# Kernel tuning notes

Hardware: AMD Instinct MI355X
Metric: run time of the kernel (lower is better)

The kernel has to match this reference:

```python
import jax, jax.numpy as jnp
import numpy as np

DIM = 2048
N_HEADS = 16
N_KV_HEADS = 4
HEAD_DIM = DIM // N_HEADS  # 128
ROPE_BASE = 10000.0
B, S = 4, 2048


def rope_tables(seq_len, head_dim, base, dtype):
    half = head_dim // 2
    inv_freq = 1.0 / (base ** (jnp.arange(0, head_dim, 2, dtype=jnp.float32) / head_dim))
    t = jnp.arange(seq_len, dtype=jnp.float32)
    freqs = jnp.outer(t, inv_freq)  # [S, half]
    return jnp.cos(freqs).astype(dtype), jnp.sin(freqs).astype(dtype)


def apply_rotary(x, cos, sin):
    # x: [B, H, S, D]; cos/sin: [S, D/2] broadcast over B,H
    half = x.shape[-1] // 2
    x1, x2 = x[..., :half], x[..., half:]
    return jnp.concatenate((x1 * cos + x2 * sin, x1 * -sin + x2 * cos), axis=-1)


def setup_inputs() -> dict:
    key = jax.random.key(0)
    ks = jax.random.split(key, 5)
    sc = 1.0 / np.sqrt(DIM)
    return {
        "x": jax.random.normal(ks[0], (B, S, DIM), dtype=jnp.float32),
        "wq": jax.random.normal(ks[1], (DIM, DIM), dtype=jnp.float32) * sc,
        "wk": jax.random.normal(ks[2], (N_KV_HEADS * HEAD_DIM, DIM), dtype=jnp.float32) * sc,
        "wv": jax.random.normal(ks[3], (N_KV_HEADS * HEAD_DIM, DIM), dtype=jnp.float32) * sc,
        "wo": jax.random.normal(ks[4], (DIM, DIM), dtype=jnp.float32) * sc,
    }


def reference(x, wq, wk, wv, wo):
    bsz, seqlen, _ = x.shape
    q = jnp.einsum("bsd,ed->bse", x, wq).reshape(bsz, seqlen, N_HEADS, HEAD_DIM).transpose(0, 2, 1, 3)
    k = jnp.einsum("bsd,ed->bse", x, wk).reshape(bsz, seqlen, N_KV_HEADS, HEAD_DIM).transpose(0, 2, 1, 3)
    v = jnp.einsum("bsd,ed->bse", x, wv).reshape(bsz, seqlen, N_KV_HEADS, HEAD_DIM).transpose(0, 2, 1, 3)

    cos, sin = rope_tables(seqlen, HEAD_DIM, ROPE_BASE, q.dtype)
    q = apply_rotary(q, cos, sin)
    k = apply_rotary(k, cos, sin)

    rep = N_HEADS // N_KV_HEADS
    if rep > 1:
        k = jnp.repeat(k, rep, axis=1)
        v = jnp.repeat(v, rep, axis=1)

    scale = 1.0 / np.sqrt(HEAD_DIM)
    logits = jnp.einsum("bhqd,bhkd->bhqk", q, k) * scale
    causal = jnp.tril(jnp.ones((seqlen, seqlen), dtype=bool))
    logits = jnp.where(causal, logits, jnp.finfo(logits.dtype).min)
    attn = jax.nn.softmax(logits, axis=-1)
    y = jnp.einsum("bhqk,bhkd->bhqd", attn, v)

    y = y.transpose(0, 2, 1, 3).reshape(bsz, seqlen, DIM)
    return jnp.einsum("bsd,ed->bse", y, wo)
```

## Files before the change

kernel.cpp:

```cpp
#include <hip/hip_runtime.h>
#include <hip/hip_bf16.h>

typedef short s16x8 __attribute__((ext_vector_type(8)));
typedef float f32x4 __attribute__((ext_vector_type(4)));
typedef float f32x16 __attribute__((ext_vector_type(16)));
typedef unsigned u32;
typedef unsigned u32x4 __attribute__((ext_vector_type(4)));
typedef unsigned short u16;

#define DMODEL 2048
#define NH     16
#define NKV    4
#define HD     128
#define NB     4
#define SS     2048

static __device__ __forceinline__ u16 f2bf(float f) {
  unsigned u = __builtin_bit_cast(unsigned, f);
  u += 0x7fffu + ((u >> 16) & 1u);
  return (u16)(u >> 16);
}
static __device__ __forceinline__ float bf2f(u16 h) {
  unsigned u = ((unsigned)h) << 16;
  return __builtin_bit_cast(float, u);
}
static __device__ __forceinline__ u32 packbf(float a, float b) {
  return (u32)f2bf(a) | ((u32)f2bf(b) << 16);
}

typedef const __attribute__((address_space(1))) void* gas_p;
typedef __attribute__((address_space(3))) void* las_p;
#define GLOAD16(g, l) __builtin_amdgcn_global_load_lds((gas_p)(const void*)(g), (las_p)(void*)(l), 16, 0, 0)

__global__ void cast_all(const float* __restrict__ x,  const float* __restrict__ wq,
                         const float* __restrict__ wk, const float* __restrict__ wv,
                         const float* __restrict__ wo,
                         u16* __restrict__ xb, u16* __restrict__ wqkv, u16* __restrict__ wob)
{
  long gid = (long)blockIdx.x * 256 + threadIdx.x;
  long i = gid * 4;
  const float* src; u16* dst; long off;
  if (i < 16777216L)       { src = x;  dst = xb;             off = i; }
  else if (i < 20971520L)  { src = wq; dst = wqkv;           off = i - 16777216L; }
  else if (i < 22020096L)  { src = wk; dst = wqkv + 4194304; off = i - 20971520L; }
  else if (i < 23068672L)  { src = wv; dst = wqkv + 5242880; off = i - 22020096L; }
  else                     { src = wo; dst = wob;            off = i - 23068672L; }
  float4 v = *(const float4*)(src + off);
  ushort4 o;
  o.x = f2bf(v.x); o.y = f2bf(v.y); o.z = f2bf(v.z); o.w = f2bf(v.w);
  *(ushort4*)(dst + off) = o;
}

static __device__ __forceinline__ void epi_store(int EPI, int row, int col, float v,
    u16* __restrict__ Oq, u16* __restrict__ Ok, u16* __restrict__ Ov, float* __restrict__ Of)
{
  if (EPI == 0) {
    int b = row >> 11, s = row & 2047;
    u16 hv = f2bf(v);
    if (col < 2048) {
      int hh = col >> 7, d = col & 127;
      Oq[(((long)(b * NH + hh)) * SS + s) * HD + d] = hv;
    } else if (col < 2560) {
      int c2 = col - 2048, kh = c2 >> 7, d = c2 & 127;
      Ok[(((long)(b * NKV + kh)) * SS + s) * HD + d] = hv;
    } else {
      int c2 = col - 2560, kh = c2 >> 7, d = c2 & 127;
      Ov[(((long)(b * NKV + kh)) * HD + d) * SS + s] = hv;
    }
  } else {
    Of[(long)row * DMODEL + col] = v;
  }
}

template<int NTC, int EPI>
__global__ __launch_bounds__(512) void gemm128(
    const u16* __restrict__ A, const u16* __restrict__ Bm, int K,
    u16* __restrict__ Oq, u16* __restrict__ Ok, u16* __restrict__ Ov, float* __restrict__ Of)
{
  __shared__ __align__(16) u16 lds[2][24576];
  const int tid = threadIdx.x, l = tid & 63, w = tid >> 6;
  const int lg = l >> 4, lr = l & 15;
  const int wm = w >> 2, wn = w & 3;

  const int nwg = NTC * 64;
  const int cpx = nwg >> 3;
  const int bid = blockIdx.x;
  const int swz = (bid & 7) * cpx + (bid >> 3);
  const int by = swz / NTC, bx = swz % NTC;
  const int rowBase = by * 128, colBase = bx * 256;

  const int rloc = w * 8 + (l >> 3);
  const int cgo  = ((l & 7) ^ (l >> 3)) * 8;
  const u16* gp[6];
#pragma unroll
  for (int seg = 0; seg < 6; seg++) {
    if (seg < 2) gp[seg] = A  + (long)(rowBase + seg * 64 + rloc) * K + cgo;
    else         gp[seg] = Bm + (long)(colBase + (seg - 2) * 64 + rloc) * K + cgo;
  }

  f32x4 acc[4][4] = {};

  auto stage = [&](int buf) {
    char* base = (char*)&lds[buf][0];
#pragma unroll
    for (int seg = 0; seg < 6; seg++)
      GLOAD16(gp[seg], base + seg * 8192 + w * 1024);
  };

  const int NKT = K >> 6;
  stage(0);
#pragma unroll
  for (int seg = 0; seg < 6; seg++) gp[seg] += 64;
  asm volatile("s_waitcnt vmcnt(0)" ::: "memory");
  __builtin_amdgcn_s_barrier();

  for (int kt = 0; kt < NKT; kt++) {
    const int cur = kt & 1;
    if (kt + 1 < NKT) {
      stage(cur ^ 1);
#pragma unroll
      for (int seg = 0; seg < 6; seg++) gp[seg] += 64;
      asm volatile("s_waitcnt vmcnt(6)" ::: "memory");
    } else {
      asm volatile("s_waitcnt vmcnt(0)" ::: "memory");
    }
    __builtin_amdgcn_s_barrier();
    asm volatile("" ::: "memory");

    const char* ab = (const char*)&lds[cur][0] + wm * 8192;
    const char* bb = (const char*)&lds[cur][0] + (2 + wn) * 8192;
    s16x8 af[4][2], bfr[4][2];
#pragma unroll
    for (int m = 0; m < 4; m++)
#pragma unroll
      for (int ks = 0; ks < 2; ks++) {
        int rr = m * 16 + lr;
        int c = ks * 4 + lg;
        af[m][ks]  = *(const s16x8*)(ab + rr * 128 + ((c ^ (rr & 7)) * 16));
        bfr[m][ks] = *(const s16x8*)(bb + rr * 128 + ((c ^ (rr & 7)) * 16));
      }
    __builtin_amdgcn_s_setprio(1);
#pragma unroll
    for (int ks = 0; ks < 2; ks++)
#pragma unroll
      for (int m = 0; m < 4; m++)
#pragma unroll
        for (int n = 0; n < 4; n++)
          acc[m][n] = __builtin_amdgcn_mfma_f32_16x16x32_bf16(af[m][ks], bfr[n][ks], acc[m][n], 0, 0, 0);
    __builtin_amdgcn_s_setprio(0);
    asm volatile("" ::: "memory");
    __builtin_amdgcn_s_barrier();
    asm volatile("" ::: "memory");
  }

#pragma unroll
  for (int m = 0; m < 4; m++)
#pragma unroll
    for (int n = 0; n < 4; n++)
#pragma unroll
      for (int r = 0; r < 4; r++)
        epi_store(EPI, rowBase + wm * 64 + m * 16 + lg * 4 + r,
                  colBase + wn * 64 + n * 16 + lr, acc[m][n][r], Oq, Ok, Ov, Of);
}

#define GPHASE(MQ, STG, WAIT)                                               \
  {                                                                         \
    s16x8 af[2][2];                                                         \
    _Pragma("unroll") for (int j = 0; j < 2; j++)                           \
      _Pragma("unroll") for (int ks = 0; ks < 2; ks++) {                    \
        int rr = (MQ) * 32 + j * 16 + lr;                                   \
        int c = ks * 4 + lg;                                                \
        af[j][ks] = *(const s16x8*)(ab + rr * 128 + ((c ^ (rr & 7)) * 16)); \
      }                                                                     \
    STG;                                                                    \
    WAIT;                                                                   \
    asm volatile("" ::: "memory");                                          \
    __builtin_amdgcn_s_barrier();                                           \
    asm volatile("" ::: "memory");                                          \
    __builtin_amdgcn_s_setprio(1);                                          \
    _Pragma("unroll") for (int ks = 0; ks < 2; ks++)                        \
      _Pragma("unroll") for (int j = 0; j < 2; j++)                         \
        _Pragma("unroll") for (int n = 0; n < 4; n++)                       \
          acc[(MQ) * 2 + j][n] = __builtin_amdgcn_mfma_f32_16x16x32_bf16(   \
              af[j][ks], bfr[n][ks], acc[(MQ) * 2 + j][n], 0, 0, 0);        \
    __builtin_amdgcn_s_setprio(0);                                          \
    asm volatile("" ::: "memory");                                          \
    __builtin_amdgcn_s_barrier();                                           \
    asm volatile("" ::: "memory");                                          \
  }

template<int NT, int EPI>
__global__ __launch_bounds__(512) void gemm256(
    const u16* __restrict__ A, const u16* __restrict__ Bm, int K,
    u16* __restrict__ Oq, u16* __restrict__ Ok, u16* __restrict__ Ov, float* __restrict__ Of)
{
  __shared__ __align__(16) u16 lds[2][32768];
  const int tid = threadIdx.x, l = tid & 63, w = tid >> 6;
  const int lg = l >> 4, lr = l & 15;
  const int wm = w >> 2, wn = w & 3;

  const int nwg = NT * 32;
  const int cpx = nwg >> 3;
  const int bid = blockIdx.x;
  const int swz = (bid & 7) * cpx + (bid >> 3);
  const int by = swz / NT, bx = swz % NT;
  const int rowBase = by * 256, colBase = bx * 256;

  const int rloc = w * 8 + (l >> 3);
  const int cgo  = ((l & 7) ^ (l >> 3)) * 8;
  const u16* gp[8];
#pragma unroll
  for (int seg = 0; seg < 8; seg++) {
    int half = (seg >> 1) & 1;
    int row  = (seg & 1) * 64 + rloc;
    if (seg < 4) gp[seg] = A  + (long)(rowBase + half * 128 + row) * K + cgo;
    else         gp[seg] = Bm + (long)(colBase + half * 128 + row) * K + cgo;
  }

  f32x4 acc[8][4] = {};

  const int NKT = K >> 6;
  {
    char* nb = (char*)&lds[0][0];
#pragma unroll
    for (int seg = 0; seg < 8; seg++)
      GLOAD16(gp[seg], nb + seg * 8192 + w * 1024);
#pragma unroll
    for (int seg = 0; seg < 8; seg++) gp[seg] += 64;
    asm volatile("s_waitcnt vmcnt(0)" ::: "memory");
    __builtin_amdgcn_s_barrier();
    asm volatile("" ::: "memory");
  }

  for (int kt = 0; kt < NKT; kt++) {
    const int cur = kt & 1;
    const bool pre = (kt + 1 < NKT);
    const char* ab = (const char*)&lds[cur][0] + wm * 16384;
    const char* bb = (const char*)&lds[cur][0] + 32768 + (wn >> 1) * 16384;
    char* nb = (char*)&lds[cur ^ 1][0];
    const int rbB = (wn & 1) * 64;

    s16x8 bfr[4][2];
#pragma unroll
    for (int n = 0; n < 4; n++)
#pragma unroll
      for (int ks = 0; ks < 2; ks++) {
        int rb = rbB + n * 16 + lr;
        int c = ks * 4 + lg;
        bfr[n][ks] = *(const s16x8*)(bb + rb * 128 + ((c ^ (rb & 7)) * 16));
      }
    GPHASE(0,
      { if (pre) { GLOAD16(gp[4], nb + 4 * 8192 + w * 1024);
                   GLOAD16(gp[5], nb + 5 * 8192 + w * 1024); } },
      { });
    GPHASE(1,
      { if (pre) { GLOAD16(gp[6], nb + 6 * 8192 + w * 1024);
                   GLOAD16(gp[7], nb + 7 * 8192 + w * 1024); } },
      { if (pre) { asm volatile("s_waitcnt vmcnt(4)" ::: "memory"); }
        else     { asm volatile("s_waitcnt vmcnt(0)" ::: "memory"); } });
    GPHASE(2,
      { if (pre) { GLOAD16(gp[0], nb + 0 * 8192 + w * 1024);
                   GLOAD16(gp[2], nb + 2 * 8192 + w * 1024); } },
      { });
    GPHASE(3,
      { if (pre) { GLOAD16(gp[1], nb + 1 * 8192 + w * 1024);
                   GLOAD16(gp[3], nb + 3 * 8192 + w * 1024); } },
      { if (pre) { asm volatile("s_waitcnt vmcnt(2)" ::: "memory"); } });

    if (pre) {
#pragma unroll
      for (int seg = 0; seg < 8; seg++) gp[seg] += 64;
    }
  }

#pragma unroll
  for (int m = 0; m < 8; m++)
#pragma unroll
    for (int n = 0; n < 4; n++)
#pragma unroll
      for (int r = 0; r < 4; r++)
        epi_store(EPI, rowBase + wm * 128 + m * 16 + lg * 4 + r,
                  colBase + wn * 64 + n * 16 + lr, acc[m][n][r], Oq, Ok, Ov, Of);
}

__global__ void rope_kernel(u16* __restrict__ Qr, u16* __restrict__ Kr)
{
  long gid = (long)blockIdx.x * 256 + threadIdx.x;
  int i = (int)(gid & 63);
  long row = gid >> 6;
  int s;
  u16* p;
  const long qrows = (long)NB * NH * SS;
  if (row < qrows) { s = (int)(row & 2047); p = Qr + row * HD; }
  else             { long r2 = row - qrows; s = (int)(r2 & 2047); p = Kr + r2 * HD; }
  float inv = exp2f(-(float)i * 0.20762050593046015f);
  float fr = (float)s * inv;
  float c = cosf(fr), sn = sinf(fr);
  float x1 = bf2f(p[i]), x2 = bf2f(p[i + 64]);
  p[i]      = f2bf(x1 * c + x2 * sn);
  p[i + 64] = f2bf(-x1 * sn + x2 * c);
}

__global__ __launch_bounds__(512) void attn_fwd(const u16* __restrict__ Qr, const u16* __restrict__ Kr,
                                                const u16* __restrict__ Vt, u16* __restrict__ Y)
{
  __shared__ __align__(16) u16 Ks[2][64 * 128];
  __shared__ __align__(16) u16 Vs[2][128 * 64];

  const int tid = threadIdx.x, l = tid & 63, w = tid >> 6;
  const int lq = l & 31, hi = l >> 5;
  const int p = blockIdx.x, h = blockIdx.y, b = blockIdx.z;
  const int kvh = h >> 2;

  const u16* Kh = Kr + ((long)(b * NKV + kvh)) * SS * HD;
  const u16* Vh = Vt + ((long)(b * NKV + kvh)) * HD * SS;
  const float scale = 0.08838834764831845f;

  auto stageK = [&](int buf, int kvb) {
    char* kb = (char*)&Ks[buf][0];
#pragma unroll
    for (int i = 0; i < 2; i++) {
      int L = w * 2048 + i * 1024 + l * 16;
      int r = L >> 8;
      int cl = (L >> 4) & 15;
      int cg = (cl & 8) | ((cl ^ r) & 7);
      GLOAD16((const char*)(Kh + (long)(kvb + r) * HD) + cg * 16, kb + w * 2048 + i * 1024);
    }
  };
  auto stageV = [&](int buf, int kvb) {
    char* vb = (char*)&Vs[buf][0];
#pragma unroll
    for (int i = 0; i < 2; i++) {
      int L = w * 2048 + i * 1024 + l * 16;
      int r = L >> 7;
      int cl = (L >> 4) & 7;
      int cg = (cl ^ r) & 7;
      GLOAD16((const char*)(Vh + (long)r * SS + kvb) + cg * 16, vb + w * 2048 + i * 1024);
    }
  };

  for (int job = 0; job < 2; job++) {
    const int qt = job ? p : 7 - p;
    const int qRow0 = qt * 256 + w * 32;
    const int qMax = qRow0 + 31;
    const int nT = 4 * qt + 4;
    const int myq = qRow0 + lq;
    const u16* Qh = Qr + (((long)(b * NH + h)) * SS + qRow0) * HD;
    u16* Yh = Y + ((long)b * SS) * DMODEL + h * HD;

    s16x8 qf[8];
#pragma unroll
    for (int kk = 0; kk < 8; kk++)
      qf[kk] = *(const s16x8*)(Qh + (long)lq * HD + kk * 16 + hi * 8);

    float m_run = -1e30f, l_run = 0.f;
    f32x16 oacc[4] = {};

    stageK(0, 0); stageV(0, 0);

    for (int t = 0; t < nT; t++) {
      const int cur = t & 1;
      if (t + 1 < nT) {
        stageK(cur ^ 1, (t + 1) * 64);
        stageV(cur ^ 1, (t + 1) * 64);
        asm volatile("s_waitcnt vmcnt(4)" ::: "memory");
      } else {
        asm volatile("s_waitcnt vmcnt(0)" ::: "memory");
      }
      __builtin_amdgcn_s_barrier();
      asm volatile("" ::: "memory");

      if (t * 64 <= qMax) {
        const char* kb = (const char*)&Ks[cur][0];
        const char* vb = (const char*)&Vs[cur][0];
        f32x16 sacc[2] = {};
#pragma unroll
        for (int kk = 0; kk < 8; kk++) {
          int ch = kk * 2 + hi;
#pragma unroll
          for (int tile = 0; tile < 2; tile++) {
            int rr = tile * 32 + lq;
            int cs = (ch & 8) | ((ch ^ rr) & 7);
            s16x8 kf = *(const s16x8*)(kb + rr * 256 + cs * 16);
            sacc[tile] = __builtin_amdgcn_mfma_f32_32x32x16_bf16(kf, qf[kk], sacc[tile], 0, 0, 0);
          }
        }
        const bool full = (t * 64 + 63 <= qRow0);
        float pmax = -1e30f;
#pragma unroll
        for (int tile = 0; tile < 2; tile++)
#pragma unroll
          for (int r = 0; r < 16; r++) {
            int kv = t * 64 + tile * 32 + (r & 3) + 8 * (r >> 2) + 4 * hi;
            float v = sacc[tile][r] * scale;
            if (!full && kv > myq) v = -30000.f;
            sacc[tile][r] = v;
            pmax = fmaxf(pmax, v);
          }
        pmax = fmaxf(pmax, __shfl_xor(pmax, 32));
        if (!__all(pmax - m_run <= 8.0f)) {
          float mnew = fmaxf(m_run, pmax);
          float sf = __expf(m_run - mnew);
          m_run = mnew; l_run *= sf;
          int sfi = __builtin_bit_cast(int, sf);
#pragma unroll
          for (int r = 0; r < 16; r++) {
            int qq = (r & 3) + 8 * (r >> 2) + 4 * hi;
            float sfr = __builtin_bit_cast(float, __builtin_amdgcn_ds_bpermute(qq << 2, sfi));
#pragma unroll
            for (int n = 0; n < 4; n++) oacc[n][r] *= sfr;
          }
        }
        float rs = 0.f;
#pragma unroll
        for (int tile = 0; tile < 2; tile++)
#pragma unroll
          for (int r = 0; r < 16; r++) {
            float pv = __expf(sacc[tile][r] - m_run);
            sacc[tile][r] = pv;
            rs += pv;
          }
        rs += __shfl_xor(rs, 32);
        l_run += rs;
        s16x8 pav[4];
#pragma unroll
        for (int tile = 0; tile < 2; tile++) {
          u32 qk[8], sw[8];
#pragma unroll
          for (int j = 0; j < 8; j++) {
            qk[j] = packbf(sacc[tile][2 * j], sacc[tile][2 * j + 1]);
            sw[j] = __shfl_xor(qk[j], 32);
          }
          u32x4 f0, f1;
          f0[0] = hi ? sw[2] : qk[0];
          f0[1] = hi ? sw[3] : qk[1];
          f0[2] = hi ? qk[2] : sw[0];
          f0[3] = hi ? qk[3] : sw[1];
          f1[0] = hi ? sw[6] : qk[4];
          f1[1] = hi ? sw[7] : qk[5];
          f1[2] = hi ? qk[6] : sw[4];
          f1[3] = hi ? qk[7] : sw[5];
          pav[tile * 2 + 0] = __builtin_bit_cast(s16x8, f0);
          pav[tile * 2 + 1] = __builtin_bit_cast(s16x8, f1);
        }
#pragma unroll
        for (int n = 0; n < 4; n++) {
          int rr = n * 32 + lq;
#pragma unroll
          for (int kk = 0; kk < 4; kk++) {
            int ch = kk * 2 + hi;
            int cs = (ch ^ rr) & 7;
            s16x8 vf = *(const s16x8*)(vb + rr * 128 + cs * 16);
            oacc[n] = __builtin_amdgcn_mfma_f32_32x32x16_bf16(pav[kk], vf, oacc[n], 0, 0, 0);
          }
        }
      }
      asm volatile("" ::: "memory");
      __builtin_amdgcn_s_barrier();
      asm volatile("" ::: "memory");
    }

    float linv = 1.f / l_run;
    int li = __builtin_bit_cast(int, linv);
#pragma unroll
    for (int r = 0; r < 16; r++) {
      int qq = (r & 3) + 8 * (r >> 2) + 4 * hi;
      float lr_ = __builtin_bit_cast(float, __builtin_amdgcn_ds_bpermute(qq << 2, li));
      u16* yrow = Yh + (long)(qRow0 + qq) * DMODEL;
#pragma unroll
      for (int n = 0; n < 4; n++)
        yrow[n * 32 + lq] = f2bf(oacc[n][r] * lr_);
    }
  }
}

extern "C" void kernel_launch(void* const* d_in, const int* in_sizes, int n_in,
                              void* d_out, int out_size, void* d_ws, size_t ws_size,
                              hipStream_t stream) {
  const float* x  = (const float*)d_in[0];
  const float* wq = (const float*)d_in[1];
  const float* wk = (const float*)d_in[2];
  const float* wv = (const float*)d_in[3];
  const float* wo = (const float*)d_in[4];
  float* out = (float*)d_out;
  char* ws = (char*)d_ws;

  u16* Xb   = (u16*)ws;
  u16* Wqkv = (u16*)(ws + 33554432);
  u16* Wob  = (u16*)(ws + 46137344);
  u16* Qr   = (u16*)(ws + 54525952);
  u16* Kr   = (u16*)(ws + 88080384);
  u16* Vt   = (u16*)(ws + 96468992);
  u16* Y    = Xb;

  cast_all<<<26624, 256, 0, stream>>>(x, wq, wk, wv, wo, Xb, Wqkv, Wob);
  gemm128<12, 0><<<768, 512, 0, stream>>>(Xb, Wqkv, DMODEL, Qr, Kr, Vt, nullptr);
  rope_kernel<<<40960, 256, 0, stream>>>(Qr, Kr);
  dim3 ag(4, NH, NB);
  attn_fwd<<<ag, 512, 0, stream>>>(Qr, Kr, Vt, Y);
  gemm256<8, 1><<<256, 512, 0, stream>>>(Y, Wob, DMODEL, nullptr, nullptr, nullptr, out);
}
```

Measured before the change: 393.9 us.

## Retile QKV GEMM to 256x128 and interleave prefetch with per-row-block MFMA phases

The QKV projection GEMM swaps its tile shape from 128 rows by 256 columns to 256 rows by 128 columns, and its warp layout from 2x4 to 4x2. The main loop is split into four phases, one per 16-row m block. Each phase issues part of the next K-tile's global-to-LDS loads, waits with a tuned vmcnt, and hits a barrier before its MFMAs. The aim is to spread memory traffic across the compute instead of issuing it all in one burst, and to cut how often the B fragment is reloaded. The cost is more barriers per K-tile and fragile hand-counted wait counts.

```diff
diff --git a/kernel.cpp b/kernel.cpp
--- a/kernel.cpp
+++ b/kernel.cpp
@@ -72,85 +72,109 @@
   }
 }
 
-template<int NTC, int EPI>
-__global__ __launch_bounds__(512) void gemm128(
+__global__ __launch_bounds__(512) void gemm_qkv(
     const u16* __restrict__ A, const u16* __restrict__ Bm, int K,
-    u16* __restrict__ Oq, u16* __restrict__ Ok, u16* __restrict__ Ov, float* __restrict__ Of)
+    u16* __restrict__ Oq, u16* __restrict__ Ok, u16* __restrict__ Ov)
 {
   __shared__ __align__(16) u16 lds[2][24576];
   const int tid = threadIdx.x, l = tid & 63, w = tid >> 6;
   const int lg = l >> 4, lr = l & 15;
-  const int wm = w >> 2, wn = w & 3;
-
-  const int nwg = NTC * 64;
+  const int wm = w >> 1, wn = w & 1;
+
+  const int NTC = 24;
+  const int nwg = 768;
   const int cpx = nwg >> 3;
   const int bid = blockIdx.x;
   const int swz = (bid & 7) * cpx + (bid >> 3);
   const int by = swz / NTC, bx = swz % NTC;
-  const int rowBase = by * 128, colBase = bx * 256;
+  const int rowBase = by * 256, colBase = bx * 128;
 
   const int rloc = w * 8 + (l >> 3);
   const int cgo  = ((l & 7) ^ (l >> 3)) * 8;
-  const u16* gp[6];
-#pragma unroll
-  for (int seg = 0; seg < 6; seg++) {
-    if (seg < 2) gp[seg] = A  + (long)(rowBase + seg * 64 + rloc) * K + cgo;
-    else         gp[seg] = Bm + (long)(colBase + (seg - 2) * 64 + rloc) * K + cgo;
-  }
+  const u16* gq[6];
+  gq[0] = Bm + (long)(colBase + rloc) * K + cgo;
+  gq[1] = Bm + (long)(colBase + 64 + rloc) * K + cgo;
+#pragma unroll
+  for (int s = 0; s < 4; s++)
+    gq[2 + s] = A + (long)(rowBase + s * 64 + rloc) * K + cgo;
+  int dst[6];
+  dst[0] = 32768 + w * 1024; dst[1] = 40960 + w * 1024;
+#pragma unroll
+  for (int s = 0; s < 4; s++) dst[2 + s] = s * 8192 + w * 1024;
 
   f32x4 acc[4][4] = {};
 
-  auto stage = [&](int buf) {
-    char* base = (char*)&lds[buf][0];
-#pragma unroll
-    for (int seg = 0; seg < 6; seg++)
-      GLOAD16(gp[seg], base + seg * 8192 + w * 1024);
-  };
-
   const int NKT = K >> 6;
-  stage(0);
-#pragma unroll
-  for (int seg = 0; seg < 6; seg++) gp[seg] += 64;
-  asm volatile("s_waitcnt vmcnt(0)" ::: "memory");
-  __builtin_amdgcn_s_barrier();
+  {
+    char* nb = (char*)&lds[0][0];
+#pragma unroll
+    for (int s = 0; s < 6; s++) GLOAD16(gq[s], nb + dst[s]);
+#pragma unroll
+    for (int s = 0; s < 6; s++) gq[s] += 64;
+    asm volatile("s_waitcnt vmcnt(0)" ::: "memory");
+    __builtin_amdgcn_s_barrier();
+    asm volatile("" ::: "memory");
+  }
 
   for (int kt = 0; kt < NKT; kt++) {
     const int cur = kt & 1;
-    if (kt + 1 < NKT) {
-      stage(cur ^ 1);
-#pragma unroll
-      for (int seg = 0; seg < 6; seg++) gp[seg] += 64;
-      asm volatile("s_waitcnt vmcnt(6)" ::: "memory");
-    } else {
-      asm volatile("s_waitcnt vmcnt(0)" ::: "memory");
-    }
-    __builtin_amdgcn_s_barrier();
-    asm volatile("" ::: "memory");
-
+    const bool pre = (kt + 1 < NKT);
     const char* ab = (const char*)&lds[cur][0] + wm * 8192;
-    const char* bb = (const char*)&lds[cur][0] + (2 + wn) * 8192;
-    s16x8 af[4][2], bfr[4][2];
-#pragma unroll
-    for (int m = 0; m < 4; m++)
+    const char* bb = (const char*)&lds[cur][0] + 32768 + wn * 8192;
+    char* nb = (char*)&lds[cur ^ 1][0];
+
+    s16x8 bfr[4][2];
+#pragma unroll
+    for (int n = 0; n < 4; n++)
+#pragma unroll
+      for (int ks = 0; ks < 2; ks++) {
+        int rb = n * 16 + lr;
+        int c = ks * 4 + lg;
+        bfr[n][ks] = *(const s16x8*)(bb + rb * 128 + ((c ^ (rb & 7)) * 16));
+      }
+
+#pragma unroll
+    for (int m = 0; m < 4; m++) {
+      s16x8 af[2];
 #pragma unroll
       for (int ks = 0; ks < 2; ks++) {
         int rr = m * 16 + lr;
         int c = ks * 4 + lg;
-        af[m][ks]  = *(const s16x8*)(ab + rr * 128 + ((c ^ (rr & 7)) * 16));
-        bfr[m][ks] = *(const s16x8*)(bb + rr * 128 + ((c ^ (rr & 7)) * 16));
+        af[ks] = *(const s16x8*)(ab + rr * 128 + ((c ^ (rr & 7)) * 16));
       }
-    __builtin_amdgcn_s_setprio(1);
-#pragma unroll
-    for (int ks = 0; ks < 2; ks++)
-#pragma unroll
-      for (int m = 0; m < 4; m++)
+      if (pre) {
+        if (m == 0)      { GLOAD16(gq[0], nb + dst[0]); GLOAD16(gq[1], nb + dst[1]);
+                           asm volatile("s_waitcnt vmcnt(4)" ::: "memory"); }
+        else if (m == 1) { GLOAD16(gq[2], nb + dst[2]); GLOAD16(gq[3], nb + dst[3]);
+                           asm volatile("s_waitcnt vmcnt(5)" ::: "memory"); }
+        else if (m == 2) { GLOAD16(gq[4], nb + dst[4]);
+                           asm volatile("s_waitcnt vmcnt(5)" ::: "memory"); }
+        else             { GLOAD16(gq[5], nb + dst[5]);
+                           asm volatile("s_waitcnt vmcnt(3)" ::: "memory"); }
+      } else {
+        if (m == 0)      { asm volatile("s_waitcnt vmcnt(2)" ::: "memory"); }
+        else if (m == 1) { asm volatile("s_waitcnt vmcnt(1)" ::: "memory"); }
+        else if (m == 2) { asm volatile("s_waitcnt vmcnt(0)" ::: "memory"); }
+      }
+      asm volatile("" ::: "memory");
+      __builtin_amdgcn_s_barrier();
+      asm volatile("" ::: "memory");
+      __builtin_amdgcn_s_setprio(1);
+#pragma unroll
+      for (int ks = 0; ks < 2; ks++)
 #pragma unroll
         for (int n = 0; n < 4; n++)
-          acc[m][n] = __builtin_amdgcn_mfma_f32_16x16x32_bf16(af[m][ks], bfr[n][ks], acc[m][n], 0, 0, 0);
-    __builtin_amdgcn_s_setprio(0);
-    asm volatile("" ::: "memory");
-    __builtin_amdgcn_s_barrier();
-    asm volatile("" ::: "memory");
+          acc[m][n] = __builtin_amdgcn_mfma_f32_16x16x32_bf16(af[ks], bfr[n][ks], acc[m][n], 0, 0, 0);
+      __builtin_amdgcn_s_setprio(0);
+      asm volatile("" ::: "memory");
+      __builtin_amdgcn_s_barrier();
+      asm volatile("" ::: "memory");
+    }
+
+    if (pre) {
+#pragma unroll
+      for (int s = 0; s < 6; s++) gq[s] += 64;
+    }
   }
 
 #pragma unroll
@@ -159,8 +183,8 @@
     for (int n = 0; n < 4; n++)
 #pragma unroll
       for (int r = 0; r < 4; r++)
-        epi_store(EPI, rowBase + wm * 64 + m * 16 + lg * 4 + r,
-                  colBase + wn * 64 + n * 16 + lr, acc[m][n][r], Oq, Ok, Ov, Of);
+        epi_store(0, rowBase + wm * 64 + m * 16 + lg * 4 + r,
+                  colBase + wn * 64 + n * 16 + lr, acc[m][n][r], Oq, Ok, Ov, nullptr);
 }
 
 #define GPHASE(MQ, STG, WAIT)                                               \
@@ -494,7 +518,7 @@
   u16* Y    = Xb;
 
   cast_all<<<26624, 256, 0, stream>>>(x, wq, wk, wv, wo, Xb, Wqkv, Wob);
-  gemm128<12, 0><<<768, 512, 0, stream>>>(Xb, Wqkv, DMODEL, Qr, Kr, Vt, nullptr);
+  gemm_qkv<<<768, 512, 0, stream>>>(Xb, Wqkv, DMODEL, Qr, Kr, Vt);
   rope_kernel<<<40960, 256, 0, stream>>>(Qr, Kr);
   dim3 ag(4, NH, NB);
   attn_fwd<<<ag, 512, 0, stream>>>(Qr, Kr, Vt, Y);
```

Result: faster. 368.0 us (-6.6%).
